# Kernel tuning notes

Measured on AMD Instinct MI355X. Metric: run time of the kernel, lower is better.

Reference implementation:

```python
import jax, jax.numpy as jnp
import numpy as np

IW = 0.2  # ratio from init


def setup_inputs() -> dict:
    key = jax.random.key(0)
    nw_out = jax.random.normal(key, (4, 19, 512, 1024), dtype=jnp.float32)
    return {"nw_out": nw_out}


def reference(nw_out) -> jnp.ndarray:
    N, C, H, W = nw_out.shape
    Np = N * H * W
    prob = jax.nn.softmax(nw_out, axis=1)                       # [N,C,H,W]
    pred = jnp.argmax(jax.lax.stop_gradient(prob), axis=1)      # [N,H,W] int
    # histogram of predicted classes (torch.histc with C bins over [0, C-1])
    hist = jnp.bincount(pred.reshape(-1), length=C).astype(prob.dtype)  # [C]
    # per-class denominator: hist^iw * Np^(1-iw), clamped to >= 1
    np_pow = jnp.asarray(Np, prob.dtype) ** (1.0 - IW)
    den_c = jnp.clip(jnp.power(hist, IW) * np_pow, 1.0)         # [C]
    den = den_c[pred][:, None, :, :]                            # [N,1,H,W] gathered, broadcasts over C
    return -jnp.sum(prob * prob / den) / (N * C)
```

## Files before the change

### kernel.cpp

```cpp
#include <hip/hip_runtime.h>
#include <math.h>

#define NC 19
#define NN 4
#define HH 512
#define WW 1024
#define NBLK 1024
#define TILES 4
#define NREP 32
#define COLS (2 * NC)
#define CSTRIDE 1024

typedef float floatx2 __attribute__((ext_vector_type(2)));

__global__ __launch_bounds__(256, 4) void msiw_pass1(const float* __restrict__ x,
                                                     float* __restrict__ ws) {
    __shared__ float s_acc[2][NREP][NC];
    const int tid = threadIdx.x;

    for (int i = tid; i < 2 * NREP * NC; i += 256) (&s_acc[0][0][0])[i] = 0.0f;
    __syncthreads();

    const size_t cs = (size_t)HH * WW;
    const int rep = tid & (NREP - 1);

    float buf[2][NC][2];

    #define TILE_BASE(r) ({                                                   \
        const int u    = (blockIdx.x * TILES + (r)) * 256 + tid;              \
        const int w2   = u & 511;                              \
        const int rest = u >> 9;                                              \
        const int h    = rest & 511;                                          \
        const int n    = rest >> 9;                                           \
        ((size_t)(n * NC) * HH + h) * WW + (size_t)w2 * 2; })

    #define LOAD_TILE(r, B)                                                   \
        {                                                                     \
            const size_t base_ = TILE_BASE(r);                                \
            _Pragma("unroll")                                                 \
            for (int c = 0; c < NC; ++c) {                                    \
                const floatx2* p2 = reinterpret_cast<const floatx2*>(         \
                    x + base_ + (size_t)c * cs);                              \
                const floatx2 v = *p2;                                        \
                buf[B][c][0] = v.x; buf[B][c][1] = v.y;                       \
            }                                                                 \
        }

    #define COMPUTE_TILE(B)                                                   \
        {                                                                     \
            float Z0 = 0.f, Z1 = 0.f, Q0 = 0.f, Q1 = 0.f;                     \
            float m0 = buf[B][0][0], m1 = buf[B][0][1];                       \
            int   p0 = 0, p1 = 0;                                             \
            _Pragma("unroll")                                                 \
            for (int c = 0; c < NC; ++c) {                                    \
                const float x0 = buf[B][c][0], x1 = buf[B][c][1];             \
                const float e0 = __expf(x0), e1 = __expf(x1);                 \
                Z0 += e0; Z1 += e1;                                           \
                Q0 = fmaf(e0, e0, Q0); Q1 = fmaf(e1, e1, Q1);                 \
                if (c > 0) {                                                  \
                    if (x0 > m0) { m0 = x0; p0 = c; }                         \
                    if (x1 > m1) { m1 = x1; p1 = c; }                         \
                }                                                             \
            }                                                                 \
            atomicAdd(&s_acc[0][rep][p0], Q0 / (Z0 * Z0));                    \
            atomicAdd(&s_acc[1][rep][p0], 1.0f);                              \
            atomicAdd(&s_acc[0][rep][p1], Q1 / (Z1 * Z1));                    \
            atomicAdd(&s_acc[1][rep][p1], 1.0f);                              \
        }

    LOAD_TILE(0, 0);
    asm volatile("" ::: "memory");
    #pragma unroll
    for (int r = 0; r < TILES - 1; ++r) {
        LOAD_TILE(r + 1, (r + 1) & 1);
        asm volatile("" ::: "memory");
        COMPUTE_TILE(r & 1);
    }
    COMPUTE_TILE((TILES - 1) & 1);

    __syncthreads();
    if (tid < COLS) {
        const int a = (tid < NC) ? 0 : 1;
        const int c = (tid < NC) ? tid : (tid - NC);
        float acc = 0.0f;
        #pragma unroll
        for (int rp = 0; rp < NREP; ++rp) acc += s_acc[a][rp][c];
        ws[(size_t)tid * CSTRIDE + blockIdx.x] = acc;
    }
}

__global__ __launch_bounds__(1024) void msiw_pass2(const float* __restrict__ ws,
                                                   float* __restrict__ out) {
    __shared__ float s_col[COLS];
    const int tid  = threadIdx.x;
    const int wv   = tid >> 6;
    const int lane = tid & 63;

    for (int col = wv; col < COLS; col += 16) {
        const float4* q = reinterpret_cast<const float4*>(ws + (size_t)col * CSTRIDE);
        float4 a[4];
        #pragma unroll
        for (int i = 0; i < 4; ++i) a[i] = q[lane + i * 64];
        float acc = 0.0f;
        #pragma unroll
        for (int i = 0; i < 4; ++i) acc += (a[i].x + a[i].y) + (a[i].z + a[i].w);
        #pragma unroll
        for (int off = 32; off > 0; off >>= 1) acc += __shfl_down(acc, off);
        if (lane == 0) s_col[col] = acc;
    }
    __syncthreads();

    if (tid == 0) {
        const double np_pow = pow((double)NN * HH * WW, 0.8);
        double total = 0.0;
        for (int c = 0; c < NC; ++c) {
            double den = pow((double)s_col[NC + c], 0.2) * np_pow;
            if (den < 1.0) den = 1.0;
            total += (double)s_col[c] / den;
        }
        out[0] = (float)(-total / (double)(NN * NC));
    }
}

extern "C" void kernel_launch(void* const* d_in, const int* in_sizes, int n_in,
                              void* d_out, int out_size, void* d_ws, size_t ws_size,
                              hipStream_t stream) {
    const float* x = (const float*)d_in[0];
    float* ws = (float*)d_ws;
    float* out = (float*)d_out;

    msiw_pass1<<<NBLK, 256, 0, stream>>>(x, ws);
    msiw_pass2<<<1, 1024, 0, stream>>>(ws, out);
}
```

Before: 46.73 us.

## Stream channel groups via global_load_lds with vmcnt-staged software pipeline

Replaces the register double-buffered per-thread loads with direct global-to-LDS asynchronous loads (global_load_lds, 16 bytes per lane), processing 4 pixels per thread in groups of 4 channels across 5 stages per tile. Manual s_waitcnt vmcnt counts and sched barriers overlap the next channel group's load with the current group's exp/argmax work, and TILES drops to 2 because each thread now covers 4 pixels. The intent is to cut register pressure and widen the memory requests so more loads stay in flight. It depends on the hand-counted vmcnt values being correct and relies only on per-wave LDS slices with no block barrier.

```diff
diff --git a/kernel.cpp b/kernel.cpp
--- a/kernel.cpp
+++ b/kernel.cpp
@@ -6,77 +6,86 @@
 #define HH 512
 #define WW 1024
 #define NBLK 1024
-#define TILES 4
+#define TILES 2
 #define NREP 32
 #define COLS (2 * NC)
 #define CSTRIDE 1024
+#define WAVES 4
 
-typedef float floatx2 __attribute__((ext_vector_type(2)));
-
-__global__ __launch_bounds__(256, 4) void msiw_pass1(const float* __restrict__ x,
-                                                     float* __restrict__ ws) {
-    __shared__ float s_acc[2][NREP][NC];
-    const int tid = threadIdx.x;
+__global__ __launch_bounds__(256) void msiw_pass1(const float* __restrict__ x,
+                                                  float* __restrict__ ws) {
+    __shared__ float4 s_tile[2][4][WAVES][64];
+    __shared__ float  s_acc[2][NREP][NC];
+    const int tid  = threadIdx.x;
+    const int wv   = tid >> 6;
+    const int lane = tid & 63;
+    const int rep  = tid & (NREP - 1);
 
     for (int i = tid; i < 2 * NREP * NC; i += 256) (&s_acc[0][0][0])[i] = 0.0f;
     __syncthreads();
 
     const size_t cs = (size_t)HH * WW;
-    const int rep = tid & (NREP - 1);
 
-    float buf[2][NC][2];
+    float Z[4], Q[4], m[4];
+    int   p[4];
 
-    #define TILE_BASE(r) ({                                                   \
-        const int u    = (blockIdx.x * TILES + (r)) * 256 + tid;              \
-        const int w2   = u & 511;                              \
-        const int rest = u >> 9;                                              \
-        const int h    = rest & 511;                                          \
-        const int n    = rest >> 9;                                           \
-        ((size_t)(n * NC) * HH + h) * WW + (size_t)w2 * 2; })
+    #define BASEPX(r) ({                                                      \
+        const int u  = ((blockIdx.x * TILES + (r)) << 8) + tid;               \
+        const int w4 = u & 255;                                               \
+        const int h  = (u >> 8) & 511;                                        \
+        const int n  = u >> 17;                                               \
+        ((size_t)(n * NC) * HH + h) * WW + (size_t)w4 * 4; })
 
-    #define LOAD_TILE(r, B)                                                   \
-        {                                                                     \
-            const size_t base_ = TILE_BASE(r);                                \
-            _Pragma("unroll")                                                 \
-            for (int c = 0; c < NC; ++c) {                                    \
-                const floatx2* p2 = reinterpret_cast<const floatx2*>(         \
-                    x + base_ + (size_t)c * cs);                              \
-                const floatx2 v = *p2;                                        \
-                buf[B][c][0] = v.x; buf[B][c][1] = v.y;                       \
-            }                                                                 \
-        }
+    #define CNTK(k) ((k) == 4 ? 3 : 4)
 
-    #define COMPUTE_TILE(B)                                                   \
-        {                                                                     \
-            float Z0 = 0.f, Z1 = 0.f, Q0 = 0.f, Q1 = 0.f;                     \
-            float m0 = buf[B][0][0], m1 = buf[B][0][1];                       \
-            int   p0 = 0, p1 = 0;                                             \
-            _Pragma("unroll")                                                 \
-            for (int c = 0; c < NC; ++c) {                                    \
-                const float x0 = buf[B][c][0], x1 = buf[B][c][1];             \
-                const float e0 = __expf(x0), e1 = __expf(x1);                 \
-                Z0 += e0; Z1 += e1;                                           \
-                Q0 = fmaf(e0, e0, Q0); Q1 = fmaf(e1, e1, Q1);                 \
-                if (c > 0) {                                                  \
-                    if (x0 > m0) { m0 = x0; p0 = c; }                         \
-                    if (x1 > m1) { m1 = x1; p1 = c; }                         \
-                }                                                             \
-            }                                                                 \
-            atomicAdd(&s_acc[0][rep][p0], Q0 / (Z0 * Z0));                    \
-            atomicAdd(&s_acc[1][rep][p0], 1.0f);                              \
-            atomicAdd(&s_acc[0][rep][p1], Q1 / (Z1 * Z1));                    \
-            atomicAdd(&s_acc[1][rep][p1], 1.0f);                              \
-        }
+    #define ISSUE(S) {                                                        \
+        const size_t bp_ = BASEPX((S) / 5);                                   \
+        _Pragma("unroll")                                                     \
+        for (int c = 0; c < CNTK((S) % 5); ++c) {                             \
+            const float* src_ = x + bp_ + (size_t)(((S) % 5) * 4 + c) * cs;   \
+            __builtin_amdgcn_global_load_lds(                                 \
+                (const __attribute__((address_space(1))) unsigned int*)src_,  \
+                (__attribute__((address_space(3))) unsigned int*)              \
+                    &s_tile[(S) & 1][c][wv][0],                               \
+                16, 0, 0);                                                    \
+        } }
 
-    LOAD_TILE(0, 0);
-    asm volatile("" ::: "memory");
-    #pragma unroll
-    for (int r = 0; r < TILES - 1; ++r) {
-        LOAD_TILE(r + 1, (r + 1) & 1);
-        asm volatile("" ::: "memory");
-        COMPUTE_TILE(r & 1);
-    }
-    COMPUTE_TILE((TILES - 1) & 1);
+    #define UPD(xv, j, ch) {                                                  \
+        const float e_ = __expf(xv);                                          \
+        if ((ch) == 0) { Z[j] = e_; Q[j] = e_ * e_; m[j] = (xv); p[j] = 0; }   \
+        else { Z[j] += e_; Q[j] = fmaf(e_, e_, Q[j]);                         \
+               if ((xv) > m[j]) { m[j] = (xv); p[j] = (ch); } } }
+
+    #define COMPUTE(S) {                                                      \
+        _Pragma("unroll")                                                     \
+        for (int c = 0; c < CNTK((S) % 5); ++c) {                             \
+            const float4 v_  = s_tile[(S) & 1][c][wv][lane];                  \
+            const int    ch_ = ((S) % 5) * 4 + c;                             \
+            UPD(v_.x, 0, ch_) UPD(v_.y, 1, ch_)                               \
+            UPD(v_.z, 2, ch_) UPD(v_.w, 3, ch_)                               \
+        } }
+
+    #define FINTILE() {                                                       \
+        _Pragma("unroll")                                                     \
+        for (int j = 0; j < 4; ++j) {                                         \
+            atomicAdd(&s_acc[0][rep][p[j]], Q[j] / (Z[j] * Z[j]));            \
+            atomicAdd(&s_acc[1][rep][p[j]], 1.0f);                            \
+        } }
+
+    #define WAITV(STR) asm volatile("s_waitcnt " STR ::: "memory");           \
+                       __builtin_amdgcn_sched_barrier(0);
+
+    ISSUE(0)
+    ISSUE(1) WAITV("vmcnt(4)") COMPUTE(0)
+    ISSUE(2) WAITV("vmcnt(4)") COMPUTE(1)
+    ISSUE(3) WAITV("vmcnt(4)") COMPUTE(2)
+    ISSUE(4) WAITV("vmcnt(3)") COMPUTE(3)
+    ISSUE(5) WAITV("vmcnt(4)") COMPUTE(4) FINTILE()
+    ISSUE(6) WAITV("vmcnt(4)") COMPUTE(5)
+    ISSUE(7) WAITV("vmcnt(4)") COMPUTE(6)
+    ISSUE(8) WAITV("vmcnt(4)") COMPUTE(7)
+    ISSUE(9) WAITV("vmcnt(3)") COMPUTE(8)
+             WAITV("vmcnt(0)") COMPUTE(9) FINTILE()
 
     __syncthreads();
     if (tid < COLS) {
```

New measurement: 55.02 us. 1.18x slower.
